# Kernel optimization log

Hardware: AMD Instinct MI355X
Metric: run time of the kernel (lower is better)

Reference implementation:

```python
import jax, jax.numpy as jnp
import numpy as np

K = 16          # neighbors per node (includes self, as in PyG knn with query==source)
EPS = 1e-5      # BatchNorm eps
B, N, C_IN = 128, 128, 6


def _bn(x, g, b):
    # BatchNorm1d in training mode: batch statistics over the leading (edge/graph) dim
    m = jnp.mean(x, axis=0)
    v = jnp.var(x, axis=0)
    return (x - m) * jax.lax.rsqrt(v + EPS) * g + b


def _edge_conv(x, W1, b1, g1, e1, W2, b2, g2, e2):
    # x: [B, N, C]. Dynamic kNN in feature space per graph, EdgeConv with max aggregation.
    Bn, Nn, C = x.shape
    sq = jnp.sum(x * x, axis=-1)                                   # [B, N]
    dist = sq[:, :, None] - 2.0 * jnp.einsum('bnc,bmc->bnm', x, x) + sq[:, None, :]
    _, idx = jax.lax.top_k(-dist, K)                               # [B, N, K]
    xj = jax.vmap(lambda xb, ib: xb[ib])(x, idx)                   # [B, N, K, C]
    xi = jnp.broadcast_to(x[:, :, None, :], xj.shape)
    e = jnp.concatenate([xi, xj - xi], axis=-1).reshape(Bn * Nn * K, 2 * C)
    h = jax.nn.relu(_bn(e @ W1 + b1, g1, e1))
    h = jax.nn.relu(_bn(h @ W2 + b2, g2, e2))
    return jnp.max(h.reshape(Bn, Nn, K, -1), axis=2)               # max-aggregate over neighbors


def setup_inputs() -> dict:
    key = jax.random.key(0)
    ks = jax.random.split(key, 16)
    s = 0.05
    d = {
        'x':   jax.random.normal(ks[0], (B, N, C_IN), jnp.float32),
        'w11': jax.random.normal(ks[1], (12, 64),  jnp.float32) * s,
        'b11': jnp.zeros((64,)),  'g11': jnp.ones((64,)),  'e11': jnp.zeros((64,)),
        'w12': jax.random.normal(ks[2], (64, 64),  jnp.float32) * s,
        'b12': jnp.zeros((64,)),  'g12': jnp.ones((64,)),  'e12': jnp.zeros((64,)),
        'w21': jax.random.normal(ks[3], (128, 128), jnp.float32) * s,
        'b21': jnp.zeros((128,)), 'g21': jnp.ones((128,)), 'e21': jnp.zeros((128,)),
        'w22': jax.random.normal(ks[4], (128, 128), jnp.float32) * s,
        'b22': jnp.zeros((128,)), 'g22': jnp.ones((128,)), 'e22': jnp.zeros((128,)),
        'w31': jax.random.normal(ks[5], (256, 256), jnp.float32) * s,
        'b31': jnp.zeros((256,)), 'g31': jnp.ones((256,)), 'e31': jnp.zeros((256,)),
        'w32': jax.random.normal(ks[6], (256, 256), jnp.float32) * s,
        'b32': jnp.zeros((256,)), 'g32': jnp.ones((256,)), 'e32': jnp.zeros((256,)),
        'fw1': jax.random.normal(ks[7], (512, 256), jnp.float32) * s,
        'fb1': jnp.zeros((256,)), 'fg1': jnp.ones((256,)), 'fe1': jnp.zeros((256,)),
        'fw2': jax.random.normal(ks[8], (256, 128), jnp.float32) * s,
        'fb2': jnp.zeros((128,)), 'fg2': jnp.ones((128,)), 'fe2': jnp.zeros((128,)),
        'fw3': jax.random.normal(ks[9], (128, 2),  jnp.float32) * s,
        'fb3': jnp.zeros((2,)),
    }
    return d


def reference(x, w11, b11, g11, e11, w12, b12, g12, e12,
              w21, b21, g21, e21, w22, b22, g22, e22,
              w31, b31, g31, e31, w32, b32, g32, e32,
              fw1, fb1, fg1, fe1, fw2, fb2, fg2, fe2, fw3, fb3):
    h = _edge_conv(x, w11, b11, g11, e11, w12, b12, g12, e12)   # [B, N, 64]
    h = _edge_conv(h, w21, b21, g21, e21, w22, b22, g22, e22)   # [B, N, 128]
    h = _edge_conv(h, w31, b31, g31, e31, w32, b32, g32, e32)   # [B, N, 256]
    pooled = jnp.concatenate([jnp.mean(h, axis=1), jnp.max(h, axis=1)], axis=-1)  # [B, 512]
    z = jax.nn.relu(_bn(pooled @ fw1 + fb1, fg1, fe1))          # dropout = identity (eval)
    z = jax.nn.relu(_bn(z @ fw2 + fb2, fg2, fe2))
    return z @ fw3 + fb3                                        # [B, 2]
```

## Files before the change

kernel.cpp:

```cpp
#include <hip/hip_runtime.h>
#include <math.h>

#define BB 128
#define NN 128
#define KK 16
#define MEDGE (BB*NN*KK)
#define MNODE (BB*NN)

typedef __bf16 bf16x8 __attribute__((ext_vector_type(8)));
typedef float  floatx4 __attribute__((ext_vector_type(4)));
typedef unsigned short u16;
typedef u16 ushort8_alias __attribute__((ext_vector_type(8)));


__device__ __forceinline__ unsigned ord32(float f) {
  unsigned u = __float_as_uint(f);
  return (u & 0x80000000u) ? ~u : (u | 0x80000000u);
}

__device__ __forceinline__ u16 bf16_rne_bits(float x) {
  unsigned u = __float_as_uint(x);
  return (u16)((u + 0x7FFF + ((u >> 16) & 1)) >> 16);
}

template<int C>
__global__ __launch_bounds__(256) void knn_fused(const float* __restrict__ x,
                                                 int* __restrict__ idx) {
  constexpr int S = C + 2;
  constexpr int DS = NN + 2;
  constexpr int XSZ = (NN * S > 64 * DS) ? NN * S : 64 * DS;
  __shared__ float xs[XSZ];
  __shared__ float sq[NN];
  int b = blockIdx.x >> 1, half = blockIdx.x & 1;
  const float* xb = x + (size_t)b * NN * C;
  int tid = threadIdx.x;

  for (int t = tid; t < NN * C; t += 256) {
    int row = t / C, c = t - row * C;
    xs[row * S + c] = xb[t];
  }
  __syncthreads();
  if (tid < NN) {
    const float* xr = xs + tid * S;
    float s = 0.f;
    for (int c = 0; c < C; ++c) s = fmaf(xr[c], xr[c], s);
    sq[tid] = s;
  }
  __syncthreads();

  int rg = tid >> 5, cg = tid & 31;
  int r0 = half * 64 + rg * 8;
  float acc[8][4];
#pragma unroll
  for (int i = 0; i < 8; ++i)
#pragma unroll
    for (int j = 0; j < 4; ++j) acc[i][j] = 0.f;
  for (int c = 0; c < C; c += 2) {
    float2 av[8], bv[4];
#pragma unroll
    for (int i = 0; i < 8; ++i) av[i] = *(const float2*)&xs[(r0 + i) * S + c];
#pragma unroll
    for (int j = 0; j < 4; ++j) bv[j] = *(const float2*)&xs[(cg + 32 * j) * S + c];
#pragma unroll
    for (int i = 0; i < 8; ++i)
#pragma unroll
      for (int j = 0; j < 4; ++j) {
        acc[i][j] = fmaf(av[i].x, bv[j].x, acc[i][j]);
        acc[i][j] = fmaf(av[i].y, bv[j].y, acc[i][j]);
      }
  }
  float dv[8][4];
#pragma unroll
  for (int i = 0; i < 8; ++i) {
    float sn = sq[r0 + i];
#pragma unroll
    for (int j = 0; j < 4; ++j) dv[i][j] = sn - 2.f * acc[i][j] + sq[cg + 32 * j];
  }
  __syncthreads();
  float* Dl = xs;
#pragma unroll
  for (int i = 0; i < 8; ++i)
#pragma unroll
    for (int j = 0; j < 4; ++j)
      Dl[(rg * 8 + i) * DS + (cg + 32 * j)] = dv[i][j];
  __syncthreads();

  int lane = tid & 63, wv = tid >> 6;
  unsigned long long lmaskLT = (1ull << lane) - 1ull;
  for (int t = 0; t < 16; ++t) {
    int lr = wv * 16 + t;
    int nd = b * NN + half * 64 + lr;
    unsigned k0 = ord32(Dl[lr * DS + lane]);
    unsigned k1 = ord32(Dl[lr * DS + lane + 64]);
    int* out = idx + (size_t)nd * KK;

    unsigned prefix = 0;
    int remaining = KK;
    int G = 2 * 64;
    int bd = 32;
    while (bd > 0) {
      --bd;
      unsigned pp = prefix << 1;
      bool m0 = (k0 >> bd) == pp;
      bool m1 = (k1 >> bd) == pp;
      int cnt0 = __popcll(__ballot(m0)) + __popcll(__ballot(m1));
      if (remaining <= cnt0) { prefix = pp; G = cnt0; }
      else                   { remaining -= cnt0; prefix = pp | 1; G -= cnt0; }
      if (G == remaining) break;
    }

    bool lt0 = (k0 >> bd) < prefix, eq0 = (k0 >> bd) == prefix;
    bool lt1 = (k1 >> bd) < prefix, eq1 = (k1 >> bd) == prefix;
    unsigned long long e0 = __ballot(eq0), e1 = __ballot(eq1);
    int c0 = __popcll(e0);
    int r0t = __popcll(e0 & lmaskLT);
    int r1t = c0 + __popcll(e1 & lmaskLT);
    bool s0 = lt0 || (eq0 && (r0t < remaining));
    bool s1 = lt1 || (eq1 && (r1t < remaining));
    unsigned long long S0 = __ballot(s0), S1 = __ballot(s1);
    int pos0 = __popcll(S0 & lmaskLT);
    int pos1 = __popcll(S0) + __popcll(S1 & lmaskLT);
    if (s0) out[pos0] = lane;
    if (s1) out[pos1] = lane + 64;
  }
}

__global__ __launch_bounds__(256) void node_gemm(const float* __restrict__ x,
                                                 const float* __restrict__ W,
                                                 float* __restrict__ p, float* __restrict__ q,
                                                 int Cin, int Cout) {
  int c = threadIdx.x;
  __shared__ float xr[128];
  for (int r = 0; r < 8; ++r) {
    int row = blockIdx.x * 8 + r;
    __syncthreads();
    for (int i = c; i < Cin; i += blockDim.x) xr[i] = x[(size_t)row * Cin + i];
    __syncthreads();
    float a = 0.f, qv = 0.f;
    for (int i = 0; i < Cin; ++i) {
      float xv = xr[i];
      a  = fmaf(xv, W[i * Cout + c], a);
      qv = fmaf(xv, W[(Cin + i) * Cout + c], qv);
    }
    p[(size_t)row * Cout + c] = a - qv;
    q[(size_t)row * Cout + c] = qv;
  }
}

template<int K, int N>
__device__ __forceinline__ void pack1_body(const float* __restrict__ W1,
                                           u16* __restrict__ Wh, u16* __restrict__ Wl,
                                           int blk, int tidx) {
  int t = blk * 256 + tidx;
  if (t >= K * N) return;
  constexpr int C = N / 2;
  constexpr int NT = N / 16;
  int j = t & 7, lane = (t >> 3) & 63, tile = t >> 9;
  int nt = tile % NT, kt = tile / NT;
  int row = kt * 32 + (lane >> 4) * 8 + j;
  int col = nt * 16 + (lane & 15);
  float w;
  if (col < C) w = W1[row * C + col] - W1[(K + row) * C + col];
  else         w = W1[(K + row) * C + (col - C)];
  u16 h = bf16_rne_bits(w);
  float hf = __uint_as_float(((unsigned)h) << 16);
  Wh[t] = h;
  Wl[t] = bf16_rne_bits(w - hf);
}

template<int C>
__device__ __forceinline__ void pack2_body(const float* __restrict__ W,
                                           u16* __restrict__ Wh, u16* __restrict__ Wl,
                                           int blk, int tidx) {
  int t = blk * 256 + tidx;
  if (t >= C * C) return;
  constexpr int NT = C / 16;
  int j = t & 7, lane = (t >> 3) & 63, tile = t >> 9;
  int nt = tile % NT, kt = tile / NT;
  int row = kt * 32 + (lane >> 4) * 8 + j;
  int col = nt * 16 + (lane & 15);
  float w = W[row * C + col];
  u16 h = bf16_rne_bits(w);
  float hf = __uint_as_float(((unsigned)h) << 16);
  Wh[t] = h;
  Wl[t] = bf16_rne_bits(w - hf);
}

__global__ __launch_bounds__(256) void pack_all(
    const float* __restrict__ w12, const float* __restrict__ w22, const float* __restrict__ w32,
    const float* __restrict__ w21, const float* __restrict__ w31,
    u16* h12, u16* l12, u16* h22, u16* l22, u16* h32, u16* l32,
    u16* h21, u16* l21, u16* h31, u16* l31) {
  int blk = blockIdx.x, tidx = threadIdx.x;
  if (blk < 16)        pack2_body<64 >(w12, h12, l12, blk,        tidx);
  else if (blk < 80)   pack2_body<128>(w22, h22, l22, blk - 16,   tidx);
  else if (blk < 336)  pack2_body<256>(w32, h32, l32, blk - 80,   tidx);
  else if (blk < 400)  pack1_body<64, 256>(w21, h21, l21, blk - 336, tidx);
  else                 pack1_body<128, 512>(w31, h31, l31, blk - 400, tidx);
}

template<int K, int N>
__global__ __launch_bounds__(512, 4) void node_gemm_v2(
    const float* __restrict__ x, const u16* __restrict__ Wh, const u16* __restrict__ Wl,
    float* __restrict__ p, float* __restrict__ q) {
  constexpr int C = N / 2;
  constexpr int KT = K / 32;
  constexpr int NT = N / 16;
  constexpr int NCOL = 64, NTS = 4;
  constexpr int NSLICE = N / 64;
  constexpr int CCH = KT * NTS * 2 * 64;
  __shared__ __align__(16) u16 Bst[CCH * 8];

  int tid = threadIdx.x, lane = tid & 63, wv = tid >> 6;
  int r = lane & 15, kseg = lane >> 4;
  int g = blockIdx.x / NSLICE, slice = blockIdx.x % NSLICE;
  int rowBase = g * 128 + wv * 16;
  const float* xr = x + (size_t)(rowBase + r) * K;

  for (int i = tid; i < CCH; i += 512) {
    int c = i & 63, h = (i >> 6) & 1, rest = i >> 7;
    int nt = rest % NTS, kt = rest / NTS;
    const ushort8_alias* src = h ? (const ushort8_alias*)Wl : (const ushort8_alias*)Wh;
    ((ushort8_alias*)Bst)[i] = src[((size_t)kt * NT + slice * NTS + nt) * 64 + c];
  }
  __syncthreads();

  floatx4 acc[NTS];
#pragma unroll
  for (int nt = 0; nt < NTS; ++nt) acc[nt] = {0.f, 0.f, 0.f, 0.f};

#pragma unroll
  for (int kt = 0; kt < KT; ++kt) {
    int c0 = kt * 32 + kseg * 8;
    float4 xa = *(const float4*)(xr + c0);
    float4 xb = *(const float4*)(xr + c0 + 4);
    float hv[8] = {xa.x, xa.y, xa.z, xa.w, xb.x, xb.y, xb.z, xb.w};
    bf16x8 ah, al;
#pragma unroll
    for (int t = 0; t < 8; ++t) {
      __bf16 hb = (__bf16)hv[t];
      ah[t] = hb;
      al[t] = (__bf16)(hv[t] - (float)hb);
    }
#pragma unroll
    for (int nt = 0; nt < NTS; ++nt) {
      int base = (kt * NTS + nt) * 128 + lane;
      bf16x8 bh = __builtin_bit_cast(bf16x8, ((const ushort8_alias*)Bst)[base]);
      bf16x8 bl = __builtin_bit_cast(bf16x8, ((const ushort8_alias*)Bst)[base + 64]);
      acc[nt] = __builtin_amdgcn_mfma_f32_16x16x32_bf16(ah, bh, acc[nt], 0, 0, 0);
      acc[nt] = __builtin_amdgcn_mfma_f32_16x16x32_bf16(al, bh, acc[nt], 0, 0, 0);
      acc[nt] = __builtin_amdgcn_mfma_f32_16x16x32_bf16(ah, bl, acc[nt], 0, 0, 0);
    }
  }

#pragma unroll
  for (int nt = 0; nt < NTS; ++nt) {
    int n = slice * NCOL + nt * 16 + r;
    float* dst = (n < C) ? p : q;
    int col = (n < C) ? n : n - C;
#pragma unroll
    for (int gi = 0; gi < 4; ++gi) {
      int row = rowBase + kseg * 4 + gi;
      dst[(size_t)row * C + col] = acc[nt][gi];
    }
  }
}

template<int C>
__global__ __launch_bounds__(256) void edge_stats1v(const float* __restrict__ p,
                                                    const float* __restrict__ q,
                                                    const float* __restrict__ b1,
                                                    const int* __restrict__ idx,
                                                    float* __restrict__ statsL) {
  constexpr int G = C / 4;
  constexpr int KL = 64 / G;
  int tid = threadIdx.x, lane = tid & 63, wv = tid >> 6;
  int nd = blockIdx.x * 4 + wv;
  int b = nd >> 7;
  int g = lane % G, kl = lane / G;
  int bank = blockIdx.x & 7;

  __shared__ float sS[C], sSS[C];
  if (tid < C) { sS[tid] = 0.f; sSS[tid] = 0.f; }
  __syncthreads();

  const float* pr = p + (size_t)nd * C;
  float4 pv = *(const float4*)(pr + g * 4);
  float4 bv = *(const float4*)(b1 + g * 4);
  pv.x += bv.x; pv.y += bv.y; pv.z += bv.z; pv.w += bv.w;
  float4 s = {0, 0, 0, 0}, ss = {0, 0, 0, 0};
  const int* id = idx + (size_t)nd * KK;
#pragma unroll
  for (int k0 = 0; k0 < KK; k0 += KL) {
    int j = id[k0 + kl];
    float4 q4 = *(const float4*)(q + (size_t)(b * NN + j) * C + g * 4);
    float y;
    y = pv.x + q4.x; s.x += y; ss.x = fmaf(y, y, ss.x);
    y = pv.y + q4.y; s.y += y; ss.y = fmaf(y, y, ss.y);
    y = pv.z + q4.z; s.z += y; ss.z = fmaf(y, y, ss.z);
    y = pv.w + q4.w; s.w += y; ss.w = fmaf(y, y, ss.w);
  }
#pragma unroll
  for (int off = G; off < 64; off <<= 1) {
    s.x += __shfl_xor(s.x, off); ss.x += __shfl_xor(ss.x, off);
    s.y += __shfl_xor(s.y, off); ss.y += __shfl_xor(ss.y, off);
    s.z += __shfl_xor(s.z, off); ss.z += __shfl_xor(ss.z, off);
    s.w += __shfl_xor(s.w, off); ss.w += __shfl_xor(ss.w, off);
  }
  if (kl == 0) {
    atomicAdd(&sS[g * 4 + 0], s.x); atomicAdd(&sSS[g * 4 + 0], ss.x);
    atomicAdd(&sS[g * 4 + 1], s.y); atomicAdd(&sSS[g * 4 + 1], ss.y);
    atomicAdd(&sS[g * 4 + 2], s.z); atomicAdd(&sSS[g * 4 + 2], ss.z);
    atomicAdd(&sS[g * 4 + 3], s.w); atomicAdd(&sSS[g * 4 + 3], ss.w);
  }
  __syncthreads();
  if (tid < C) {
    atomicAdd(&statsL[bank * 256 + tid], sS[tid]);
    atomicAdd(&statsL[2048 + bank * 256 + tid], sSS[tid]);
  }
}

template<int C, int NCOL, int CK, int MPN>
__global__ __launch_bounds__(512, 4) void edge_gemm2_v13(
    const float* __restrict__ p, const float* __restrict__ q,
    const int* __restrict__ idx,
    const float* __restrict__ statsL,
    const float* __restrict__ g1, const float* __restrict__ e1,
    const float* __restrict__ b1,
    const u16* __restrict__ Wh, const u16* __restrict__ Wl,
    const float* __restrict__ b2,
    float* __restrict__ zmax, float* __restrict__ zmin,
    float* __restrict__ s2b, float* __restrict__ ss2b) {
  constexpr int KT = C / 32;
  constexpr int NT = C / 16;
  constexpr int NSLICE = C / NCOL;
  constexpr int NTS = NCOL / 16;
  constexpr int NWIN = KT / CK;
  constexpr int CCH = CK * NTS * 2 * 64;
  constexpr int NPB = 8 * MPN;
  constexpr int GPB = NN / NPB;
  __shared__ __align__(16) u16 Bst[CCH * 8];
  __shared__ float sScl[C], sShf[C];
  __shared__ float sS[NCOL], sSS[NCOL];

  int tid = threadIdx.x, lane = tid & 63, wv = tid >> 6;
  int r = lane & 15, kseg = lane >> 4;

  int g = blockIdx.x / NSLICE, slice = blockIdx.x % NSLICE;
  int u = g >> 3, xcd = g & 7;
  int b = xcd + 8 * (u / GPB);
  int nodeBase = b * NN + (u % GPB) * NPB;

  if (tid < C) {
    float s = 0.f, ssum = 0.f;
#pragma unroll
    for (int k = 0; k < 8; ++k) {
      s += statsL[k * 256 + tid];
      ssum += statsL[2048 + k * 256 + tid];
    }
    float mean = s / (float)MEDGE;
    float var = ssum / (float)MEDGE - mean * mean;
    if (var < 0.f) var = 0.f;
    float sc = g1[tid] * rsqrtf(var + 1e-5f);
    sScl[tid] = sc;
    sShf[tid] = e1[tid] - mean * sc + sc * b1[tid];
  }
  if (tid < NCOL) { sS[tid] = 0.f; sSS[tid] = 0.f; }

  int nd[MPN];
  const float *pr[MPN], *qr[MPN];
#pragma unroll
  for (int m = 0; m < MPN; ++m) {
    nd[m] = nodeBase + wv * MPN + m;
    int j = idx[(size_t)nd[m] * KK + r];
    pr[m] = p + (size_t)nd[m] * C;
    qr[m] = q + (size_t)(b * NN + j) * C;
  }

  floatx4 acc[MPN][NTS];
#pragma unroll
  for (int nt = 0; nt < NTS; ++nt) {
    float bv = b2[slice * NCOL + nt * 16 + r];
#pragma unroll
    for (int m = 0; m < MPN; ++m) acc[m][nt] = {bv, bv, bv, bv};
  }

#pragma unroll
  for (int w = 0; w < NWIN; ++w) {
    if (w > 0) __syncthreads();
    for (int i = tid; i < CCH; i += 512) {
      int c = i & 63, h = (i >> 6) & 1, rest = i >> 7;
      int nt = rest % NTS, kk = rest / NTS;
      const ushort8_alias* src = h ? (const ushort8_alias*)Wl : (const ushort8_alias*)Wh;
      ((ushort8_alias*)Bst)[i] = src[((size_t)(w * CK + kk) * NT + slice * NTS + nt) * 64 + c];
    }
    __syncthreads();

#pragma unroll
    for (int kk = 0; kk < CK; ++kk) {
      int c0 = (w * CK + kk) * 32 + kseg * 8;
      float4 sa = *(const float4*)(sScl + c0);
      float4 sb = *(const float4*)(sScl + c0 + 4);
      float4 ta = *(const float4*)(sShf + c0);
      float4 tb = *(const float4*)(sShf + c0 + 4);
      bf16x8 ah[MPN], al[MPN];
#pragma unroll
      for (int m = 0; m < MPN; ++m) {
        float4 pa = *(const float4*)(pr[m] + c0);
        float4 pb = *(const float4*)(pr[m] + c0 + 4);
        float4 qa = *(const float4*)(qr[m] + c0);
        float4 qb = *(const float4*)(qr[m] + c0 + 4);
        float hv[8];
        hv[0] = fmaxf(fmaf(pa.x + qa.x, sa.x, ta.x), 0.f);
        hv[1] = fmaxf(fmaf(pa.y + qa.y, sa.y, ta.y), 0.f);
        hv[2] = fmaxf(fmaf(pa.z + qa.z, sa.z, ta.z), 0.f);
        hv[3] = fmaxf(fmaf(pa.w + qa.w, sa.w, ta.w), 0.f);
        hv[4] = fmaxf(fmaf(pb.x + qb.x, sb.x, tb.x), 0.f);
        hv[5] = fmaxf(fmaf(pb.y + qb.y, sb.y, tb.y), 0.f);
        hv[6] = fmaxf(fmaf(pb.z + qb.z, sb.z, tb.z), 0.f);
        hv[7] = fmaxf(fmaf(pb.w + qb.w, sb.w, tb.w), 0.f);
#pragma unroll
        for (int t = 0; t < 8; ++t) {
          __bf16 hb = (__bf16)hv[t];
          ah[m][t] = hb;
          al[m][t] = (__bf16)(hv[t] - (float)hb);
        }
      }
#pragma unroll
      for (int nt = 0; nt < NTS; ++nt) {
        int base = (kk * NTS + nt) * 128 + lane;
        bf16x8 bh = __builtin_bit_cast(bf16x8, ((const ushort8_alias*)Bst)[base]);
        bf16x8 bl = __builtin_bit_cast(bf16x8, ((const ushort8_alias*)Bst)[base + 64]);
#pragma unroll
        for (int m = 0; m < MPN; ++m) {
          acc[m][nt] = __builtin_amdgcn_mfma_f32_16x16x32_bf16(ah[m], bh, acc[m][nt], 0, 0, 0);
          acc[m][nt] = __builtin_amdgcn_mfma_f32_16x16x32_bf16(al[m], bh, acc[m][nt], 0, 0, 0);
          acc[m][nt] = __builtin_amdgcn_mfma_f32_16x16x32_bf16(ah[m], bl, acc[m][nt], 0, 0, 0);
        }
      }
    }
  }

  int bank = blockIdx.x & 7;
#pragma unroll
  for (int m = 0; m < MPN; ++m) {
#pragma unroll
    for (int nt = 0; nt < NTS; ++nt) {
      float s = 0.f, ss = 0.f, mx = -INFINITY, mn = INFINITY;
#pragma unroll
      for (int gi = 0; gi < 4; ++gi) {
        float z = acc[m][nt][gi];
        s += z; ss = fmaf(z, z, ss);
        mx = fmaxf(mx, z); mn = fminf(mn, z);
      }
      mx = fmaxf(mx, __shfl_xor(mx, 16)); mn = fminf(mn, __shfl_xor(mn, 16));
      s += __shfl_xor(s, 16); ss += __shfl_xor(ss, 16);
      mx = fmaxf(mx, __shfl_xor(mx, 32)); mn = fminf(mn, __shfl_xor(mn, 32));
      s += __shfl_xor(s, 32); ss += __shfl_xor(ss, 32);
      if (kseg == 0) {
        int colL = nt * 16 + r;
        int col = slice * NCOL + colL;
        zmax[(size_t)nd[m] * C + col] = mx;
        zmin[(size_t)nd[m] * C + col] = mn;
        atomicAdd(&sS[colL], s);
        atomicAdd(&sSS[colL], ss);
      }
    }
  }
  __syncthreads();
  if (tid < NCOL) {
    atomicAdd(&s2b[bank * 256 + slice * NCOL + tid], sS[tid]);
    atomicAdd(&ss2b[bank * 256 + slice * NCOL + tid], sSS[tid]);
  }
}

__global__ __launch_bounds__(256) void finalize2_kernel(const float* __restrict__ zmax,
                                                        const float* __restrict__ zmin,
                                                        const float* __restrict__ s2b,
                                                        const float* __restrict__ ss2b,
                                                        const float* __restrict__ g2,
                                                        const float* __restrict__ e2,
                                                        float* __restrict__ out, int Cmask) {
  int t = blockIdx.x * 256 + threadIdx.x;
  int c = t & Cmask;
  float s = 0.f, ss = 0.f;
#pragma unroll
  for (int k = 0; k < 8; ++k) {
    s += s2b[k * 256 + c];
    ss += ss2b[k * 256 + c];
  }
  float mean = s / (float)MEDGE;
  float var = ss / (float)MEDGE - mean * mean;
  if (var < 0.f) var = 0.f;
  float scl = g2[c] * rsqrtf(var + 1e-5f);
  float shf = e2[c] - mean * scl;
  float v = (scl >= 0.f) ? zmax[t] : zmin[t];
  out[t] = fmaxf(fmaf(v, scl, shf), 0.f);
}

__global__ __launch_bounds__(256) void fin3_pool(const float* __restrict__ zmax,
                                                 const float* __restrict__ zmin,
                                                 const float* __restrict__ s2b,
                                                 const float* __restrict__ ss2b,
                                                 const float* __restrict__ g2,
                                                 const float* __restrict__ e2,
                                                 float* __restrict__ pooled) {
  int b = blockIdx.x >> 2, cc = blockIdx.x & 3;
  int tid = threadIdx.x;
  int cl = tid & 63, ng = tid >> 6;
  int c = cc * 64 + cl;
  float s = 0.f, ss = 0.f;
#pragma unroll
  for (int k = 0; k < 8; ++k) { s += s2b[k * 256 + c]; ss += ss2b[k * 256 + c]; }
  float mean = s / (float)MEDGE;
  float var = ss / (float)MEDGE - mean * mean;
  if (var < 0.f) var = 0.f;
  float scl = g2[c] * rsqrtf(var + 1e-5f);
  float shf = e2[c] - mean * scl;

  float acc = 0.f, mx = -INFINITY;
  for (int n = ng * 32; n < ng * 32 + 32; ++n) {
    size_t t = (size_t)(b * NN + n) * 256 + c;
    float vx = zmax[t], vn = zmin[t];
    float v = (scl >= 0.f) ? vx : vn;
    float h = fmaxf(fmaf(v, scl, shf), 0.f);
    acc += h; mx = fmaxf(mx, h);
  }
  __shared__ float sSum[4][64], sMax[4][64];
  sSum[ng][cl] = acc; sMax[ng][cl] = mx;
  __syncthreads();
  if (ng == 0) {
    float a = sSum[0][cl] + sSum[1][cl] + sSum[2][cl] + sSum[3][cl];
    float m = fmaxf(fmaxf(sMax[0][cl], sMax[1][cl]), fmaxf(sMax[2][cl], sMax[3][cl]));
    pooled[b * 512 + c] = a * (1.f / 128.f);
    pooled[b * 512 + 256 + c] = m;
  }
}

__global__ __launch_bounds__(256) void fc1_fused(const float* __restrict__ pooled,
                                                 const float* __restrict__ W,
                                                 const float* __restrict__ bias,
                                                 float* __restrict__ t1raw,
                                                 float* __restrict__ fs, float* __restrict__ fss) {
  int b = blockIdx.x, c = threadIdx.x;
  __shared__ float row[512];
  row[c] = pooled[b * 512 + c];
  row[c + 256] = pooled[b * 512 + 256 + c];
  __syncthreads();
  float acc = bias[c];
  for (int i = 0; i < 512; ++i) acc = fmaf(row[i], W[i * 256 + c], acc);
  t1raw[b * 256 + c] = acc;
  atomicAdd(&fs[c], acc);
  atomicAdd(&fss[c], acc * acc);
}

__global__ __launch_bounds__(256) void fc2_fused(const float* __restrict__ t1raw,
                                                 const float* __restrict__ fs,
                                                 const float* __restrict__ fss,
                                                 const float* __restrict__ g1,
                                                 const float* __restrict__ e1,
                                                 const float* __restrict__ W,
                                                 const float* __restrict__ bias,
                                                 float* __restrict__ t2raw,
                                                 float* __restrict__ gs, float* __restrict__ gss) {
  int b = blockIdx.x, c = threadIdx.x;
  __shared__ float row[256];
  {
    float mean = fs[c] / 128.f;
    float var = fss[c] / 128.f - mean * mean;
    if (var < 0.f) var = 0.f;
    float scl = g1[c] * rsqrtf(var + 1e-5f);
    float shf = e1[c] - mean * scl;
    row[c] = fmaxf(fmaf(t1raw[b * 256 + c], scl, shf), 0.f);
  }
  __syncthreads();
  if (c < 128) {
    float acc = bias[c];
    for (int i = 0; i < 256; ++i) acc = fmaf(row[i], W[i * 128 + c], acc);
    t2raw[b * 128 + c] = acc;
    atomicAdd(&gs[c], acc);
    atomicAdd(&gss[c], acc * acc);
  }
}

__global__ __launch_bounds__(256) void fc3_fused(const float* __restrict__ t2raw,
                                                 const float* __restrict__ gs,
                                                 const float* __restrict__ gss,
                                                 const float* __restrict__ g2,
                                                 const float* __restrict__ e2,
                                                 const float* __restrict__ W,
                                                 const float* __restrict__ bias,
                                                 float* __restrict__ out) {
  __shared__ float row[128 * 2];
  int t = threadIdx.x;
  if (t < 128) {
    float mean = gs[t] / 128.f;
    float var = gss[t] / 128.f - mean * mean;
    if (var < 0.f) var = 0.f;
    float scl = g2[t] * rsqrtf(var + 1e-5f);
    row[t] = scl;
    row[128 + t] = e2[t] - mean * scl;
  }
  __syncthreads();
  int b = t >> 1, jj = t & 1;
  float acc = bias[jj];
  for (int r = 0; r < 128; ++r) {
    float v = fmaxf(fmaf(t2raw[b * 128 + r], row[r], row[128 + r]), 0.f);
    acc = fmaf(v, W[r * 2 + jj], acc);
  }
  out[t] = acc;
}


struct LayerPtrs {
  int* idx; float *p, *q, *zmx, *zmn;
};

template<int Cin, int C, bool DOFIN>
static void run_edgeconv(const float* xin,
                         const float* W1, const float* b1, const float* g1, const float* e1,
                         const float* b2, const float* g2, const float* e2,
                         const u16* Wh1, const u16* Wl1, const u16* Wh2, const u16* Wl2,
                         float* hout, float* statsL, const LayerPtrs& L, hipStream_t stream) {
  float* s2b = statsL + 4096;
  float* ss2b = statsL + 6144;

  knn_fused<Cin><<<dim3(BB * 2), dim3(256), 0, stream>>>(xin, L.idx);
  if constexpr (Cin >= 16) {
    constexpr int NSL1 = (2 * C) / 64;
    node_gemm_v2<Cin, 2 * C><<<dim3((MNODE / 128) * NSL1), dim3(512), 0, stream>>>(
        xin, Wh1, Wl1, L.p, L.q);
  } else {
    node_gemm<<<dim3(MNODE / 8), dim3(C), 0, stream>>>(xin, W1, L.p, L.q, Cin, C);
  }
  edge_stats1v<C><<<dim3(MNODE / 4), dim3(256), 0, stream>>>(L.p, L.q, b1, L.idx, statsL);
  constexpr int NCOL = (C == 256) ? 128 : C;
  constexpr int CKW = (C == 64) ? 2 : 4;
  constexpr int MPN = 2;
  constexpr int NSL = C / NCOL;
  edge_gemm2_v13<C, NCOL, CKW, MPN><<<dim3((MNODE / (8 * MPN)) * NSL), dim3(512), 0, stream>>>(
      L.p, L.q, L.idx, statsL, g1, e1, b1, Wh2, Wl2, b2, L.zmx, L.zmn, s2b, ss2b);
  if constexpr (DOFIN) {
    finalize2_kernel<<<dim3(MNODE * C / 256), dim3(256), 0, stream>>>(
        L.zmx, L.zmn, s2b, ss2b, g2, e2, hout, C - 1);
  }
}


extern "C" void kernel_launch(void* const* d_in, const int* in_sizes, int n_in,
                              void* d_out, int out_size, void* d_ws, size_t ws_size,
                              hipStream_t stream) {
  const float* x   = (const float*)d_in[0];
  const float* w11 = (const float*)d_in[1];
  const float* b11 = (const float*)d_in[2];
  const float* g11 = (const float*)d_in[3];
  const float* e11 = (const float*)d_in[4];
  const float* w12 = (const float*)d_in[5];
  const float* b12 = (const float*)d_in[6];
  const float* g12 = (const float*)d_in[7];
  const float* e12 = (const float*)d_in[8];
  const float* w21 = (const float*)d_in[9];
  const float* b21 = (const float*)d_in[10];
  const float* g21 = (const float*)d_in[11];
  const float* e21 = (const float*)d_in[12];
  const float* w22 = (const float*)d_in[13];
  const float* b22 = (const float*)d_in[14];
  const float* g22 = (const float*)d_in[15];
  const float* e22 = (const float*)d_in[16];
  const float* w31 = (const float*)d_in[17];
  const float* b31 = (const float*)d_in[18];
  const float* g31 = (const float*)d_in[19];
  const float* e31 = (const float*)d_in[20];
  const float* w32 = (const float*)d_in[21];
  const float* b32 = (const float*)d_in[22];
  const float* g32 = (const float*)d_in[23];
  const float* e32 = (const float*)d_in[24];
  const float* fw1 = (const float*)d_in[25];
  const float* fb1 = (const float*)d_in[26];
  const float* fg1 = (const float*)d_in[27];
  const float* fe1 = (const float*)d_in[28];
  const float* fw2 = (const float*)d_in[29];
  const float* fb2 = (const float*)d_in[30];
  const float* fg2 = (const float*)d_in[31];
  const float* fe2 = (const float*)d_in[32];
  const float* fw3 = (const float*)d_in[33];
  const float* fb3 = (const float*)d_in[34];

  char* wsb = (char*)d_ws;
  size_t o = 0;
  auto alloc = [&](size_t bytes) -> void* {
    void* r = wsb + o;
    o += (bytes + 255) & ~(size_t)255;
    return r;
  };
  LayerPtrs L;
  L.idx   = (int*)  alloc((size_t)MNODE * KK * sizeof(int));
  L.p     = (float*)alloc((size_t)MNODE * 256 * sizeof(float));
  L.q     = (float*)alloc((size_t)MNODE * 256 * sizeof(float));
  L.zmx   = (float*)alloc((size_t)MNODE * 256 * sizeof(float));
  L.zmn   = (float*)alloc((size_t)MNODE * 256 * sizeof(float));
  u16* h12 = (u16*)alloc(64 * 64 * sizeof(u16));
  u16* l12 = (u16*)alloc(64 * 64 * sizeof(u16));
  u16* h22 = (u16*)alloc(128 * 128 * sizeof(u16));
  u16* l22 = (u16*)alloc(128 * 128 * sizeof(u16));
  u16* h32 = (u16*)alloc(256 * 256 * sizeof(u16));
  u16* l32 = (u16*)alloc(256 * 256 * sizeof(u16));
  u16* h21 = (u16*)alloc(64 * 256 * sizeof(u16));
  u16* l21 = (u16*)alloc(64 * 256 * sizeof(u16));
  u16* h31 = (u16*)alloc(128 * 512 * sizeof(u16));
  u16* l31 = (u16*)alloc(128 * 512 * sizeof(u16));
  float* statsAll = (float*)alloc((3 * 8192 + 1024) * sizeof(float));
  float* h1buf   = (float*)alloc((size_t)MNODE * 64 * sizeof(float));
  float* h2buf   = (float*)alloc((size_t)MNODE * 128 * sizeof(float));
  float* pooled  = (float*)alloc(128 * 512 * sizeof(float));
  float* t1raw   = (float*)alloc(128 * 256 * sizeof(float));
  float* t2raw   = (float*)alloc(128 * 128 * sizeof(float));

  float* fcstats = statsAll + 3 * 8192;
  float* fs  = fcstats;
  float* fss = fcstats + 256;
  float* gs  = fcstats + 512;
  float* gss = fcstats + 768;

  (void)hipMemsetAsync(statsAll, 0, (3 * 8192 + 1024) * sizeof(float), stream);
  pack_all<<<dim3(656), dim3(256), 0, stream>>>(w12, w22, w32, w21, w31,
      h12, l12, h22, l22, h32, l32, h21, l21, h31, l31);

  run_edgeconv<6, 64, true>(x, w11, b11, g11, e11, b12, g12, e12,
                            nullptr, nullptr, h12, l12,
                            h1buf, statsAll, L, stream);
  run_edgeconv<64, 128, true>(h1buf, nullptr, b21, g21, e21, b22, g22, e22,
                              h21, l21, h22, l22,
                              h2buf, statsAll + 8192, L, stream);
  run_edgeconv<128, 256, false>(h2buf, nullptr, b31, g31, e31, b32, g32, e32,
                                h31, l31, h32, l32,
                                nullptr, statsAll + 16384, L, stream);

  {
    float* s2b3 = statsAll + 16384 + 4096;
    float* ss2b3 = statsAll + 16384 + 6144;
    fin3_pool<<<dim3(BB * 4), dim3(256), 0, stream>>>(L.zmx, L.zmn, s2b3, ss2b3,
                                                      g32, e32, pooled);
  }
  fc1_fused<<<dim3(BB), dim3(256), 0, stream>>>(pooled, fw1, fb1, t1raw, fs, fss);
  fc2_fused<<<dim3(BB), dim3(256), 0, stream>>>(t1raw, fs, fss, fg1, fe1, fw2, fb2, t2raw, gs, gss);
  fc3_fused<<<dim3(1), dim3(256), 0, stream>>>(t2raw, gs, gss, fg2, fe2, fw3, fb3, (float*)d_out);
}
```

Measured before the change: 627.2 us.

## Pre-apply BN1 scale to p/q in separate pass; software-pipeline edge GEMM loads

```diff
diff --git a/kernel.cpp b/kernel.cpp
--- a/kernel.cpp
+++ b/kernel.cpp
@@ -320,13 +320,52 @@
   }
 }
 
-template<int C, int NCOL, int CK, int MPN>
-__global__ __launch_bounds__(512, 4) void edge_gemm2_v13(
+template<int C>
+__global__ __launch_bounds__(256) void bn_finalize(const float* __restrict__ statsL,
+                                                   const float* __restrict__ g1,
+                                                   const float* __restrict__ e1,
+                                                   const float* __restrict__ b1,
+                                                   float* __restrict__ scl,
+                                                   float* __restrict__ shf) {
+  int c = threadIdx.x;
+  if (c >= C) return;
+  float s = 0.f, ss = 0.f;
+#pragma unroll
+  for (int k = 0; k < 8; ++k) {
+    s += statsL[k * 256 + c];
+    ss += statsL[2048 + k * 256 + c];
+  }
+  float mean = s / (float)MEDGE;
+  float var = ss / (float)MEDGE - mean * mean;
+  if (var < 0.f) var = 0.f;
+  float sc = g1[c] * rsqrtf(var + 1e-5f);
+  scl[c] = sc;
+  shf[c] = e1[c] - mean * sc + sc * b1[c];
+}
+
+template<int C>
+__global__ __launch_bounds__(256) void bn_apply(float* __restrict__ p,
+                                                float* __restrict__ q,
+                                                const float* __restrict__ scl,
+                                                const float* __restrict__ shf) {
+  int t = blockIdx.x * 256 + threadIdx.x;
+  int i4 = t * 4;
+  int c = i4 & (C - 1);
+  float4 sc = *(const float4*)(scl + c);
+  float4 sh = *(const float4*)(shf + c);
+  float4 pv = *(const float4*)(p + i4);
+  pv.x = fmaf(pv.x, sc.x, sh.x); pv.y = fmaf(pv.y, sc.y, sh.y);
+  pv.z = fmaf(pv.z, sc.z, sh.z); pv.w = fmaf(pv.w, sc.w, sh.w);
+  *(float4*)(p + i4) = pv;
+  float4 qv = *(const float4*)(q + i4);
+  qv.x *= sc.x; qv.y *= sc.y; qv.z *= sc.z; qv.w *= sc.w;
+  *(float4*)(q + i4) = qv;
+}
+
+template<int C, int NCOL, int CK>
+__global__ __launch_bounds__(512, 4) void edge_gemm2_v14(
     const float* __restrict__ p, const float* __restrict__ q,
     const int* __restrict__ idx,
-    const float* __restrict__ statsL,
-    const float* __restrict__ g1, const float* __restrict__ e1,
-    const float* __restrict__ b1,
     const u16* __restrict__ Wh, const u16* __restrict__ Wl,
     const float* __restrict__ b2,
     float* __restrict__ zmax, float* __restrict__ zmin,
@@ -337,10 +376,7 @@
   constexpr int NTS = NCOL / 16;
   constexpr int NWIN = KT / CK;
   constexpr int CCH = CK * NTS * 2 * 64;
-  constexpr int NPB = 8 * MPN;
-  constexpr int GPB = NN / NPB;
   __shared__ __align__(16) u16 Bst[CCH * 8];
-  __shared__ float sScl[C], sShf[C];
   __shared__ float sS[NCOL], sSS[NCOL];
 
   int tid = threadIdx.x, lane = tid & 63, wv = tid >> 6;
@@ -348,42 +384,53 @@
 
   int g = blockIdx.x / NSLICE, slice = blockIdx.x % NSLICE;
   int u = g >> 3, xcd = g & 7;
-  int b = xcd + 8 * (u / GPB);
-  int nodeBase = b * NN + (u % GPB) * NPB;
-
-  if (tid < C) {
-    float s = 0.f, ssum = 0.f;
-#pragma unroll
-    for (int k = 0; k < 8; ++k) {
-      s += statsL[k * 256 + tid];
-      ssum += statsL[2048 + k * 256 + tid];
-    }
-    float mean = s / (float)MEDGE;
-    float var = ssum / (float)MEDGE - mean * mean;
-    if (var < 0.f) var = 0.f;
-    float sc = g1[tid] * rsqrtf(var + 1e-5f);
-    sScl[tid] = sc;
-    sShf[tid] = e1[tid] - mean * sc + sc * b1[tid];
-  }
+  int b = xcd + 8 * (u >> 4);
+  int nd = b * NN + (u & 15) * 8 + wv;
+
   if (tid < NCOL) { sS[tid] = 0.f; sSS[tid] = 0.f; }
 
-  int nd[MPN];
-  const float *pr[MPN], *qr[MPN];
-#pragma unroll
-  for (int m = 0; m < MPN; ++m) {
-    nd[m] = nodeBase + wv * MPN + m;
-    int j = idx[(size_t)nd[m] * KK + r];
-    pr[m] = p + (size_t)nd[m] * C;
-    qr[m] = q + (size_t)(b * NN + j) * C;
-  }
-
-  floatx4 acc[MPN][NTS];
+  int j = idx[(size_t)nd * KK + r];
+  const float* pr = p + (size_t)nd * C;
+  const float* qr = q + (size_t)(b * NN + j) * C;
+
+  floatx4 acc[NTS];
 #pragma unroll
   for (int nt = 0; nt < NTS; ++nt) {
     float bv = b2[slice * NCOL + nt * 16 + r];
-#pragma unroll
-    for (int m = 0; m < MPN; ++m) acc[m][nt] = {bv, bv, bv, bv};
-  }
+    acc[nt] = {bv, bv, bv, bv};
+  }
+
+  float4 pA0, pA1, qA0, qA1;
+  float4 pB0, pB1, qB0, qB1;
+
+#define EG_LOAD(P0, P1, Q0, Q1, T) do { int c0_ = (T) * 32 + kseg * 8; \
+    P0 = *(const float4*)(pr + c0_); P1 = *(const float4*)(pr + c0_ + 4); \
+    Q0 = *(const float4*)(qr + c0_); Q1 = *(const float4*)(qr + c0_ + 4); } while (0)
+
+#define EG_COMPUTE(P0, P1, Q0, Q1, KKI) do { \
+    float h_[8]; \
+    h_[0] = fmaxf(P0.x + Q0.x, 0.f); h_[1] = fmaxf(P0.y + Q0.y, 0.f); \
+    h_[2] = fmaxf(P0.z + Q0.z, 0.f); h_[3] = fmaxf(P0.w + Q0.w, 0.f); \
+    h_[4] = fmaxf(P1.x + Q1.x, 0.f); h_[5] = fmaxf(P1.y + Q1.y, 0.f); \
+    h_[6] = fmaxf(P1.z + Q1.z, 0.f); h_[7] = fmaxf(P1.w + Q1.w, 0.f); \
+    bf16x8 ah, al; \
+    _Pragma("unroll") \
+    for (int t_ = 0; t_ < 8; ++t_) { \
+      __bf16 hb_ = (__bf16)h_[t_]; \
+      ah[t_] = hb_; \
+      al[t_] = (__bf16)(h_[t_] - (float)hb_); \
+    } \
+    _Pragma("unroll") \
+    for (int nt_ = 0; nt_ < NTS; ++nt_) { \
+      int base_ = ((KKI) * NTS + nt_) * 128 + lane; \
+      bf16x8 bh_ = __builtin_bit_cast(bf16x8, ((const ushort8_alias*)Bst)[base_]); \
+      bf16x8 bl_ = __builtin_bit_cast(bf16x8, ((const ushort8_alias*)Bst)[base_ + 64]); \
+      acc[nt_] = __builtin_amdgcn_mfma_f32_16x16x32_bf16(ah, bh_, acc[nt_], 0, 0, 0); \
+      acc[nt_] = __builtin_amdgcn_mfma_f32_16x16x32_bf16(al, bh_, acc[nt_], 0, 0, 0); \
+      acc[nt_] = __builtin_amdgcn_mfma_f32_16x16x32_bf16(ah, bl_, acc[nt_], 0, 0, 0); \
+    } } while (0)
+
+  EG_LOAD(pA0, pA1, qA0, qA1, 0);
 
 #pragma unroll
   for (int w = 0; w < NWIN; ++w) {
@@ -397,74 +444,40 @@
     __syncthreads();
 
 #pragma unroll
-    for (int kk = 0; kk < CK; ++kk) {
-      int c0 = (w * CK + kk) * 32 + kseg * 8;
-      float4 sa = *(const float4*)(sScl + c0);
-      float4 sb = *(const float4*)(sScl + c0 + 4);
-      float4 ta = *(const float4*)(sShf + c0);
-      float4 tb = *(const float4*)(sShf + c0 + 4);
-      bf16x8 ah[MPN], al[MPN];
-#pragma unroll
-      for (int m = 0; m < MPN; ++m) {
-        float4 pa = *(const float4*)(pr[m] + c0);
-        float4 pb = *(const float4*)(pr[m] + c0 + 4);
-        float4 qa = *(const float4*)(qr[m] + c0);
-        float4 qb = *(const float4*)(qr[m] + c0 + 4);
-        float hv[8];
-        hv[0] = fmaxf(fmaf(pa.x + qa.x, sa.x, ta.x), 0.f);
-        hv[1] = fmaxf(fmaf(pa.y + qa.y, sa.y, ta.y), 0.f);
-        hv[2] = fmaxf(fmaf(pa.z + qa.z, sa.z, ta.z), 0.f);
-        hv[3] = fmaxf(fmaf(pa.w + qa.w, sa.w, ta.w), 0.f);
-        hv[4] = fmaxf(fmaf(pb.x + qb.x, sb.x, tb.x), 0.f);
-        hv[5] = fmaxf(fmaf(pb.y + qb.y, sb.y, tb.y), 0.f);
-        hv[6] = fmaxf(fmaf(pb.z + qb.z, sb.z, tb.z), 0.f);
-        hv[7] = fmaxf(fmaf(pb.w + qb.w, sb.w, tb.w), 0.f);
-#pragma unroll
-        for (int t = 0; t < 8; ++t) {
-          __bf16 hb = (__bf16)hv[t];
-          ah[m][t] = hb;
-          al[m][t] = (__bf16)(hv[t] - (float)hb);
-        }
-      }
-#pragma unroll
-      for (int nt = 0; nt < NTS; ++nt) {
-        int base = (kk * NTS + nt) * 128 + lane;
-        bf16x8 bh = __builtin_bit_cast(bf16x8, ((const ushort8_alias*)Bst)[base]);
-        bf16x8 bl = __builtin_bit_cast(bf16x8, ((const ushort8_alias*)Bst)[base + 64]);
-#pragma unroll
-        for (int m = 0; m < MPN; ++m) {
-          acc[m][nt] = __builtin_amdgcn_mfma_f32_16x16x32_bf16(ah[m], bh, acc[m][nt], 0, 0, 0);
-          acc[m][nt] = __builtin_amdgcn_mfma_f32_16x16x32_bf16(al[m], bh, acc[m][nt], 0, 0, 0);
-          acc[m][nt] = __builtin_amdgcn_mfma_f32_16x16x32_bf16(ah[m], bl, acc[m][nt], 0, 0, 0);
-        }
-      }
-    }
-  }
+    for (int kp = 0; kp < CK; kp += 2) {
+      int t1 = w * CK + kp + 1;
+      EG_LOAD(pB0, pB1, qB0, qB1, t1);
+      EG_COMPUTE(pA0, pA1, qA0, qA1, kp);
+      int t2 = w * CK + kp + 2;
+      if (t2 >= KT) t2 = 0;
+      EG_LOAD(pA0, pA1, qA0, qA1, t2);
+      EG_COMPUTE(pB0, pB1, qB0, qB1, kp + 1);
+    }
+  }
+#undef EG_LOAD
+#undef EG_COMPUTE
 
   int bank = blockIdx.x & 7;
 #pragma unroll
-  for (int m = 0; m < MPN; ++m) {
-#pragma unroll
-    for (int nt = 0; nt < NTS; ++nt) {
-      float s = 0.f, ss = 0.f, mx = -INFINITY, mn = INFINITY;
-#pragma unroll
-      for (int gi = 0; gi < 4; ++gi) {
-        float z = acc[m][nt][gi];
-        s += z; ss = fmaf(z, z, ss);
-        mx = fmaxf(mx, z); mn = fminf(mn, z);
-      }
-      mx = fmaxf(mx, __shfl_xor(mx, 16)); mn = fminf(mn, __shfl_xor(mn, 16));
-      s += __shfl_xor(s, 16); ss += __shfl_xor(ss, 16);
-      mx = fmaxf(mx, __shfl_xor(mx, 32)); mn = fminf(mn, __shfl_xor(mn, 32));
-      s += __shfl_xor(s, 32); ss += __shfl_xor(ss, 32);
-      if (kseg == 0) {
-        int colL = nt * 16 + r;
-        int col = slice * NCOL + colL;
-        zmax[(size_t)nd[m] * C + col] = mx;
-        zmin[(size_t)nd[m] * C + col] = mn;
-        atomicAdd(&sS[colL], s);
-        atomicAdd(&sSS[colL], ss);
-      }
+  for (int nt = 0; nt < NTS; ++nt) {
+    float s = 0.f, ss = 0.f, mx = -INFINITY, mn = INFINITY;
+#pragma unroll
+    for (int gi = 0; gi < 4; ++gi) {
+      float z = acc[nt][gi];
+      s += z; ss = fmaf(z, z, ss);
+      mx = fmaxf(mx, z); mn = fminf(mn, z);
+    }
+    mx = fmaxf(mx, __shfl_xor(mx, 16)); mn = fminf(mn, __shfl_xor(mn, 16));
+    s += __shfl_xor(s, 16); ss += __shfl_xor(ss, 16);
+    mx = fmaxf(mx, __shfl_xor(mx, 32)); mn = fminf(mn, __shfl_xor(mn, 32));
+    s += __shfl_xor(s, 32); ss += __shfl_xor(ss, 32);
+    if (kseg == 0) {
+      int colL = nt * 16 + r;
+      int col = slice * NCOL + colL;
+      zmax[(size_t)nd * C + col] = mx;
+      zmin[(size_t)nd * C + col] = mn;
+      atomicAdd(&sS[colL], s);
+      atomicAdd(&sSS[colL], ss);
     }
   }
   __syncthreads();
@@ -614,6 +627,7 @@
 
 struct LayerPtrs {
   int* idx; float *p, *q, *zmx, *zmn;
+  float *scl, *shf;
 };
 
 template<int Cin, int C, bool DOFIN>
@@ -634,12 +648,13 @@
     node_gemm<<<dim3(MNODE / 8), dim3(C), 0, stream>>>(xin, W1, L.p, L.q, Cin, C);
   }
   edge_stats1v<C><<<dim3(MNODE / 4), dim3(256), 0, stream>>>(L.p, L.q, b1, L.idx, statsL);
-  constexpr int NCOL = (C == 256) ? 128 : C;
+  bn_finalize<C><<<dim3(1), dim3(256), 0, stream>>>(statsL, g1, e1, b1, L.scl, L.shf);
+  bn_apply<C><<<dim3(MNODE * C / 1024), dim3(256), 0, stream>>>(L.p, L.q, L.scl, L.shf);
+  constexpr int NCOL = (C == 64) ? 64 : 128;
   constexpr int CKW = (C == 64) ? 2 : 4;
-  constexpr int MPN = 2;
   constexpr int NSL = C / NCOL;
-  edge_gemm2_v13<C, NCOL, CKW, MPN><<<dim3((MNODE / (8 * MPN)) * NSL), dim3(512), 0, stream>>>(
-      L.p, L.q, L.idx, statsL, g1, e1, b1, Wh2, Wl2, b2, L.zmx, L.zmn, s2b, ss2b);
+  edge_gemm2_v14<C, NCOL, CKW><<<dim3((MNODE / 8) * NSL), dim3(512), 0, stream>>>(
+      L.p, L.q, L.idx, Wh2, Wl2, b2, L.zmx, L.zmn, s2b, ss2b);
   if constexpr (DOFIN) {
     finalize2_kernel<<<dim3(MNODE * C / 256), dim3(256), 0, stream>>>(
         L.zmx, L.zmn, s2b, ss2b, g2, e2, hout, C - 1);
@@ -699,6 +714,8 @@
   L.q     = (float*)alloc((size_t)MNODE * 256 * sizeof(float));
   L.zmx   = (float*)alloc((size_t)MNODE * 256 * sizeof(float));
   L.zmn   = (float*)alloc((size_t)MNODE * 256 * sizeof(float));
+  L.scl   = (float*)alloc(256 * sizeof(float));
+  L.shf   = (float*)alloc(256 * sizeof(float));
   u16* h12 = (u16*)alloc(64 * 64 * sizeof(u16));
   u16* l12 = (u16*)alloc(64 * 64 * sizeof(u16));
   u16* h22 = (u16*)alloc(128 * 128 * sizeof(u16));
```

Result: slower. 665.6 us (+6.1%).

## Add persistent 1024-thread edge GEMM kernel staging full weight slice in LDS

Applied to the files above, without the earlier changes.

```diff
diff --git a/kernel.cpp b/kernel.cpp
--- a/kernel.cpp
+++ b/kernel.cpp
@@ -474,6 +474,159 @@
   }
 }
 
+template<int C, int NCOL, int MPN, int BLKS>
+__global__ __launch_bounds__(1024, 4) void edge_gemm2_v16(
+    const float* __restrict__ p, const float* __restrict__ q,
+    const int* __restrict__ idx,
+    const float* __restrict__ statsL,
+    const float* __restrict__ g1, const float* __restrict__ e1,
+    const float* __restrict__ b1,
+    const u16* __restrict__ Wh, const u16* __restrict__ Wl,
+    const float* __restrict__ b2,
+    float* __restrict__ zmax, float* __restrict__ zmin,
+    float* __restrict__ s2b, float* __restrict__ ss2b) {
+  constexpr int KT = C / 32;
+  constexpr int NT = C / 16;
+  constexpr int NSLICE = C / NCOL;
+  constexpr int NTS = NCOL / 16;
+  constexpr int CCH = KT * NTS * 2 * 64;
+  constexpr int NPG = 16 * MPN;
+  constexpr int ITER = MNODE / NPG / BLKS;
+  __shared__ __align__(16) u16 Bst[CCH * 8];
+  __shared__ float sScl[C], sShf[C];
+  __shared__ float sS[NCOL], sSS[NCOL];
+
+  int tid = threadIdx.x, lane = tid & 63, wv = tid >> 6;
+  int r = lane & 15, kseg = lane >> 4;
+  int blk = blockIdx.x / NSLICE, slice = blockIdx.x % NSLICE;
+
+  if (tid < C) {
+    float s = 0.f, ssum = 0.f;
+#pragma unroll
+    for (int k = 0; k < 8; ++k) {
+      s += statsL[k * 256 + tid];
+      ssum += statsL[2048 + k * 256 + tid];
+    }
+    float mean = s / (float)MEDGE;
+    float var = ssum / (float)MEDGE - mean * mean;
+    if (var < 0.f) var = 0.f;
+    float sc = g1[tid] * rsqrtf(var + 1e-5f);
+    sScl[tid] = sc;
+    sShf[tid] = e1[tid] - mean * sc + sc * b1[tid];
+  }
+  if (tid < NCOL) { sS[tid] = 0.f; sSS[tid] = 0.f; }
+
+  for (int i = tid; i < CCH; i += 1024) {
+    int c = i & 63, h = (i >> 6) & 1, rest = i >> 7;
+    int nt = rest % NTS, kt = rest / NTS;
+    const ushort8_alias* src = h ? (const ushort8_alias*)Wl : (const ushort8_alias*)Wh;
+    ((ushort8_alias*)Bst)[i] = src[((size_t)kt * NT + slice * NTS + nt) * 64 + c];
+  }
+  __syncthreads();
+
+#pragma unroll 1
+  for (int it = 0; it < ITER; ++it) {
+    int group = blk * ITER + it;
+    int nodeBase = group * NPG + wv * MPN;
+
+    int nd[MPN];
+    const float *pr[MPN], *qr[MPN];
+#pragma unroll
+    for (int m = 0; m < MPN; ++m) {
+      nd[m] = nodeBase + m;
+      int b = nd[m] >> 7;
+      int j = idx[(size_t)nd[m] * KK + r];
+      pr[m] = p + (size_t)nd[m] * C;
+      qr[m] = q + (size_t)(b * NN + j) * C;
+    }
+
+    floatx4 acc[MPN][NTS];
+#pragma unroll
+    for (int nt = 0; nt < NTS; ++nt) {
+      float bv = b2[slice * NCOL + nt * 16 + r];
+#pragma unroll
+      for (int m = 0; m < MPN; ++m) acc[m][nt] = {bv, bv, bv, bv};
+    }
+
+#pragma unroll
+    for (int kk = 0; kk < KT; ++kk) {
+      int c0 = kk * 32 + kseg * 8;
+      float4 sa = *(const float4*)(sScl + c0);
+      float4 sb = *(const float4*)(sScl + c0 + 4);
+      float4 ta = *(const float4*)(sShf + c0);
+      float4 tb = *(const float4*)(sShf + c0 + 4);
+      bf16x8 ah[MPN], al[MPN];
+#pragma unroll
+      for (int m = 0; m < MPN; ++m) {
+        float4 pa = *(const float4*)(pr[m] + c0);
+        float4 pb = *(const float4*)(pr[m] + c0 + 4);
+        float4 qa = *(const float4*)(qr[m] + c0);
+        float4 qb = *(const float4*)(qr[m] + c0 + 4);
+        float hv[8];
+        hv[0] = fmaxf(fmaf(pa.x + qa.x, sa.x, ta.x), 0.f);
+        hv[1] = fmaxf(fmaf(pa.y + qa.y, sa.y, ta.y), 0.f);
+        hv[2] = fmaxf(fmaf(pa.z + qa.z, sa.z, ta.z), 0.f);
+        hv[3] = fmaxf(fmaf(pa.w + qa.w, sa.w, ta.w), 0.f);
+        hv[4] = fmaxf(fmaf(pb.x + qb.x, sb.x, tb.x), 0.f);
+        hv[5] = fmaxf(fmaf(pb.y + qb.y, sb.y, tb.y), 0.f);
+        hv[6] = fmaxf(fmaf(pb.z + qb.z, sb.z, tb.z), 0.f);
+        hv[7] = fmaxf(fmaf(pb.w + qb.w, sb.w, tb.w), 0.f);
+#pragma unroll
+        for (int t = 0; t < 8; ++t) {
+          __bf16 hb = (__bf16)hv[t];
+          ah[m][t] = hb;
+          al[m][t] = (__bf16)(hv[t] - (float)hb);
+        }
+      }
+#pragma unroll
+      for (int nt = 0; nt < NTS; ++nt) {
+        int base = (kk * NTS + nt) * 128 + lane;
+        bf16x8 bh = __builtin_bit_cast(bf16x8, ((const ushort8_alias*)Bst)[base]);
+        bf16x8 bl = __builtin_bit_cast(bf16x8, ((const ushort8_alias*)Bst)[base + 64]);
+#pragma unroll
+        for (int m = 0; m < MPN; ++m) {
+          acc[m][nt] = __builtin_amdgcn_mfma_f32_16x16x32_bf16(ah[m], bh, acc[m][nt], 0, 0, 0);
+          acc[m][nt] = __builtin_amdgcn_mfma_f32_16x16x32_bf16(al[m], bh, acc[m][nt], 0, 0, 0);
+          acc[m][nt] = __builtin_amdgcn_mfma_f32_16x16x32_bf16(ah[m], bl, acc[m][nt], 0, 0, 0);
+        }
+      }
+    }
+
+#pragma unroll
+    for (int m = 0; m < MPN; ++m) {
+#pragma unroll
+      for (int nt = 0; nt < NTS; ++nt) {
+        float s = 0.f, ss = 0.f, mx = -INFINITY, mn = INFINITY;
+#pragma unroll
+        for (int gi = 0; gi < 4; ++gi) {
+          float z = acc[m][nt][gi];
+          s += z; ss = fmaf(z, z, ss);
+          mx = fmaxf(mx, z); mn = fminf(mn, z);
+        }
+        mx = fmaxf(mx, __shfl_xor(mx, 16)); mn = fminf(mn, __shfl_xor(mn, 16));
+        s += __shfl_xor(s, 16); ss += __shfl_xor(ss, 16);
+        mx = fmaxf(mx, __shfl_xor(mx, 32)); mn = fminf(mn, __shfl_xor(mn, 32));
+        s += __shfl_xor(s, 32); ss += __shfl_xor(ss, 32);
+        if (kseg == 0) {
+          int colL = nt * 16 + r;
+          int col = slice * NCOL + colL;
+          zmax[(size_t)nd[m] * C + col] = mx;
+          zmin[(size_t)nd[m] * C + col] = mn;
+          atomicAdd(&sS[colL], s);
+          atomicAdd(&sSS[colL], ss);
+        }
+      }
+    }
+  }
+
+  __syncthreads();
+  int bank = blockIdx.x & 7;
+  if (tid < NCOL) {
+    atomicAdd(&s2b[bank * 256 + slice * NCOL + tid], sS[tid]);
+    atomicAdd(&ss2b[bank * 256 + slice * NCOL + tid], sSS[tid]);
+  }
+}
+
 __global__ __launch_bounds__(256) void finalize2_kernel(const float* __restrict__ zmax,
                                                         const float* __restrict__ zmin,
                                                         const float* __restrict__ s2b,
@@ -634,12 +787,17 @@
     node_gemm<<<dim3(MNODE / 8), dim3(C), 0, stream>>>(xin, W1, L.p, L.q, Cin, C);
   }
   edge_stats1v<C><<<dim3(MNODE / 4), dim3(256), 0, stream>>>(L.p, L.q, b1, L.idx, statsL);
-  constexpr int NCOL = (C == 256) ? 128 : C;
-  constexpr int CKW = (C == 64) ? 2 : 4;
-  constexpr int MPN = 2;
-  constexpr int NSL = C / NCOL;
-  edge_gemm2_v13<C, NCOL, CKW, MPN><<<dim3((MNODE / (8 * MPN)) * NSL), dim3(512), 0, stream>>>(
-      L.p, L.q, L.idx, statsL, g1, e1, b1, Wh2, Wl2, b2, L.zmx, L.zmn, s2b, ss2b);
+  if constexpr (C == 64) {
+    edge_gemm2_v13<64, 64, 2, 2><<<dim3(MNODE / 16), dim3(512), 0, stream>>>(
+        L.p, L.q, L.idx, statsL, g1, e1, b1, Wh2, Wl2, b2, L.zmx, L.zmn, s2b, ss2b);
+  } else {
+    constexpr int NCOL = 128;
+    constexpr int MPN = 2;
+    constexpr int BLKS = (C == 256) ? 128 : 256;
+    constexpr int NSL = C / NCOL;
+    edge_gemm2_v16<C, NCOL, MPN, BLKS><<<dim3(NSL * BLKS), dim3(1024), 0, stream>>>(
+        L.p, L.q, L.idx, statsL, g1, e1, b1, Wh2, Wl2, b2, L.zmx, L.zmn, s2b, ss2b);
+  }
   if constexpr (DOFIN) {
     finalize2_kernel<<<dim3(MNODE * C / 256), dim3(256), 0, stream>>>(
         L.zmx, L.zmn, s2b, ss2b, g2, e2, hout, C - 1);
```

New measurement: 2.039 ms. 3.25x slower.
